# Kernel tuning notes

Hardware: AMD Instinct MI355X
Metric: run time of the kernel (lower is better)

Reference implementation:

```python
import jax, jax.numpy as jnp
import numpy as np

NUM_HEADS = 16  # config.num_attention_heads


def setup_inputs() -> dict:
    key = jax.random.key(0)
    k0, k1, k2 = jax.random.split(key, 3)
    B, S, D = 2, 2048, 2048
    hd = D // NUM_HEADS  # 128
    hidden_states = jax.random.normal(k0, (B, S, D), dtype=jnp.float32)
    c_attn_w = jax.random.normal(k1, (D + 2 * hd, D), dtype=jnp.float32) * 0.02
    c_attn_b = jnp.zeros((D + 2 * hd,), dtype=jnp.float32)
    c_proj_w = jax.random.normal(k2, (D, D), dtype=jnp.float32) * 0.02
    c_proj_b = jnp.zeros((D,), dtype=jnp.float32)
    return {
        "hidden_states": hidden_states,
        "c_attn_w": c_attn_w,
        "c_attn_b": c_attn_b,
        "c_proj_w": c_proj_w,
        "c_proj_b": c_proj_b,
    }


def reference(hidden_states, c_attn_w, c_attn_b, c_proj_w, c_proj_b):
    B, S, D = hidden_states.shape
    H = NUM_HEADS
    hd = D // H
    scale = hd ** -0.5

    # fused QKV projection: [B,S,D] -> [B,S,D+2*hd]
    qkv = hidden_states @ c_attn_w.T + c_attn_b
    # multi-query split: per-head Q, single shared K and V
    q = qkv[..., :D].reshape(B, S, H, hd)        # [B,S,H,hd]
    k = qkv[..., D:D + hd]                       # [B,S,hd]
    v = qkv[..., D + hd:]                        # [B,S,hd]

    # attention scores (full matrix materialized, like the baddbmm path)
    scores = jnp.einsum('bqhd,bkd->bhqk', q, k) * scale  # [B,H,S,S]
    causal = jnp.tril(jnp.ones((S, S), dtype=bool))
    scores = jnp.where(causal, scores, jnp.finfo(scores.dtype).min)
    attn = jax.nn.softmax(scores, axis=-1)

    # context: shared V broadcast across heads
    ctx = jnp.einsum('bhqk,bkd->bqhd', attn, v).reshape(B, S, D)
    out = ctx @ c_proj_w.T + c_proj_b
    return out
```

## Files before the change

kernel.cpp:

```cpp
#include <hip/hip_runtime.h>
#include <hip/hip_bf16.h>
#include <math.h>

typedef unsigned short u16;
typedef __attribute__((ext_vector_type(8))) __bf16 bf16x8;
typedef __attribute__((ext_vector_type(4))) float f32x4;

__device__ inline u16 f2bf(float f) {
  union { float f; unsigned u; } x; x.f = f;
  unsigned r = x.u + 0x7fffu + ((x.u >> 16) & 1u);
  return (u16)(r >> 16);
}

__device__ inline unsigned cvtpk(float lo, float hi) {
  unsigned r;
  asm("v_cvt_pk_bf16_f32 %0, %1, %2" : "=v"(r) : "v"(lo), "v"(hi));
  return r;
}

__device__ inline float fexp2(float x) {
  float r;
  asm("v_exp_f32 %0, %1" : "=v"(r) : "v"(x));
  return r;
}

__device__ inline void async16(const void* g, void* l) {
  __builtin_amdgcn_global_load_lds(
      (const __attribute__((address_space(1))) void*)g,
      (__attribute__((address_space(3))) void*)l, 16, 0, 0);
}

__global__ __launch_bounds__(256) void cast3_kernel(
    const float* __restrict__ hs, const float* __restrict__ aw,
    const float* __restrict__ pw, u16* __restrict__ hs_o,
    u16* __restrict__ aw_o, u16* __restrict__ pw_o) {
  int blk = blockIdx.x;
  const float* in;
  u16* out;
  int i;
  if (blk < 8192) {
    in = hs; out = hs_o; i = blk * 256 + threadIdx.x;
  } else if (blk < 12800) {
    in = aw; out = aw_o; i = (blk - 8192) * 256 + threadIdx.x;
  } else {
    in = pw; out = pw_o; i = (blk - 12800) * 256 + threadIdx.x;
  }
  float4 v = ((const float4*)in)[i];
  u16 o0 = f2bf(v.x), o1 = f2bf(v.y), o2 = f2bf(v.z), o3 = f2bf(v.w);
  unsigned lo = (unsigned)o0 | ((unsigned)o1 << 16);
  unsigned hi = (unsigned)o2 | ((unsigned)o3 << 16);
  ((uint2*)out)[i] = make_uint2(lo, hi);
}

__global__ __launch_bounds__(256) void vt_kernel(
    const u16* __restrict__ qkv, u16* __restrict__ vt) {
  __shared__ u16 tile[32][136];
  const int t = threadIdx.x;
  const int b = blockIdx.x >> 6;
  const int S0 = (blockIdx.x & 63) * 32;
  const int s_l = t >> 3, dg = t & 7;
  const u16* src = qkv + ((size_t)b * 2048 + S0 + s_l) * 2304 + 2176 + dg * 16;
  *(uint4*)&tile[s_l][dg * 16] = *(const uint4*)src;
  *(uint4*)&tile[s_l][dg * 16 + 8] = *(const uint4*)(src + 8);
  __syncthreads();
  const int d = t >> 1, sh = t & 1;
  u16 buf[16];
#pragma unroll
  for (int j = 0; j < 16; ++j) buf[j] = tile[sh * 16 + j][d];
  u16* dst = vt + ((size_t)b * 128 + d) * 2048 + S0 + sh * 16;
  *(uint4*)dst = *(uint4*)&buf[0];
  *(uint4*)(dst + 8) = *(uint4*)&buf[8];
}

template <bool BF16OUT>
__global__ __launch_bounds__(256) void gemm_bt(
    const u16* __restrict__ A, const u16* __restrict__ Bw,
    const float* __restrict__ bias, void* __restrict__ Cout,
    int M, int N, int K, int qcols, float qscale) {
  __shared__ u16 As[2][128 * 64];
  __shared__ u16 Bs[2][128 * 64];
  const int t = threadIdx.x;
  const int w = t >> 6;
  const int lane = t & 63;
  const int lq = lane >> 4, lr = lane & 15;

  int bx = blockIdx.x, by = blockIdx.y;
  const int gx = gridDim.x, gy = gridDim.y;
  if ((gx & 1) == 0 && (gy & 3) == 0) {
    const int cw = gx >> 1, ch = gy >> 2;
    int id = by * gx + bx;
    int xcd = id & 7, j = id >> 3;
    bx = (xcd & 1) * cw + j % cw;
    by = (xcd >> 1) * ch + j / cw;
  }

  const long brow = (long)by * 128;
  const long bcol = (long)bx * 128;
  const int wr = (w >> 1) * 64, wc = (w & 1) * 64;
  f32x4 acc[4][4] = {};

  int rA[4], cA[4];
#pragma unroll
  for (int it = 0; it < 4; ++it) {
    int ci = it * 256 + t;
    rA[it] = ci >> 3;
    cA[it] = (ci & 7) ^ (rA[it] & 7);
  }

  char* const AsB = (char*)&As[0][0];
  char* const BsB = (char*)&Bs[0][0];

  auto stage = [&](int buf, int kt) {
    char* ad = AsB + buf * 16384;
    char* bd = BsB + buf * 16384;
#pragma unroll
    for (int it = 0; it < 4; ++it) {
      const u16* srcA = A + (brow + rA[it]) * (long)K + kt + cA[it] * 8;
      async16(srcA, ad + (it * 256 + w * 64) * 16);
      const u16* srcB = Bw + (bcol + rA[it]) * (long)K + kt + cA[it] * 8;
      async16(srcB, bd + (it * 256 + w * 64) * 16);
    }
  };

  const int swz = ((lr & 4) << 4) + ((lq << 4) ^ ((lr & 3) << 4));
  const int aB0 = (wr + lr) * 128 + swz;
  const int bB0 = (wc + lr) * 128 + swz;
  const char* const a00 = AsB + aB0;
  const char* const a01 = AsB + (aB0 ^ 64);
  const char* const a10 = AsB + 16384 + aB0;
  const char* const a11 = AsB + 16384 + (aB0 ^ 64);
  const char* const b00 = BsB + bB0;
  const char* const b01 = BsB + (bB0 ^ 64);
  const char* const b10 = BsB + 16384 + bB0;
  const char* const b11 = BsB + 16384 + (bB0 ^ 64);

  auto computeK = [&](const char* a0, const char* a1, const char* b0,
                      const char* b1) {
    bf16x8 af[4], bfr[4];
#pragma unroll
    for (int m = 0; m < 4; ++m) af[m] = *(const bf16x8*)(a0 + m * 2048);
#pragma unroll
    for (int n = 0; n < 4; ++n) bfr[n] = *(const bf16x8*)(b0 + n * 2048);
#pragma unroll
    for (int m = 0; m < 4; ++m)
#pragma unroll
      for (int n = 0; n < 4; ++n)
        acc[m][n] = __builtin_amdgcn_mfma_f32_16x16x32_bf16(
            af[m], bfr[n], acc[m][n], 0, 0, 0);
#pragma unroll
    for (int m = 0; m < 4; ++m) af[m] = *(const bf16x8*)(a1 + m * 2048);
#pragma unroll
    for (int n = 0; n < 4; ++n) bfr[n] = *(const bf16x8*)(b1 + n * 2048);
#pragma unroll
    for (int m = 0; m < 4; ++m)
#pragma unroll
      for (int n = 0; n < 4; ++n)
        acc[m][n] = __builtin_amdgcn_mfma_f32_16x16x32_bf16(
            af[m], bfr[n], acc[m][n], 0, 0, 0);
  };

  stage(0, 0);
  __syncthreads();

  for (int kt = 0; kt < K; kt += 128) {
    if (kt + 64 < K) stage(1, kt + 64);
    computeK(a00, a01, b00, b01);
    __syncthreads();
    if (kt + 128 < K) stage(0, kt + 128);
    computeK(a10, a11, b10, b11);
    __syncthreads();
  }

#pragma unroll
  for (int m = 0; m < 4; ++m) {
    long row0 = brow + wr + m * 16 + lq * 4;
#pragma unroll
    for (int n = 0; n < 4; ++n) {
      long col = bcol + wc + n * 16 + lr;
      float bv = bias[col];
      float cs = (col < qcols) ? qscale : 1.f;
#pragma unroll
      for (int j = 0; j < 4; ++j) {
        float v = (acc[m][n][j] + bv) * cs;
        if (BF16OUT)
          ((u16*)Cout)[(row0 + j) * N + col] = f2bf(v);
        else
          ((float*)Cout)[(row0 + j) * N + col] = v;
      }
    }
  }
}

__global__ __launch_bounds__(256, 2) void attn_kernel(
    const u16* __restrict__ qkv, const u16* __restrict__ vt,
    u16* __restrict__ ctx) {
  __shared__ u16 Kl[2][64 * 136];
  __shared__ u16 Vl[2][128 * 72];
  __shared__ u16 Pl[4][16 * 72];

  const int t = threadIdx.x;
  const int w = t >> 6;
  const int lane = t & 63;
  const int lq = lane >> 4, lr = lane & 15;
  const int lkey = lq * 4;
  const int bid = blockIdx.x;
  const int qtid = bid >> 5;
  const int qt = (qtid < 8) ? (15 - qtid) : (qtid - 8);
  const int hb = bid & 31;
  const int h = hb & 15;
  const int b = hb >> 4;
  const int s0w = qt * 128 + w * 32;
  const size_t qb = (size_t)b * 2048 * 2304;

  bf16x8 qg[2][4];
#pragma unroll
  for (int s = 0; s < 2; ++s)
#pragma unroll
    for (int kc = 0; kc < 4; ++kc)
      qg[s][kc] = *(const bf16x8*)(qkv + qb +
                                   (size_t)(s0w + s * 16 + lr) * 2304 +
                                   h * 128 + kc * 32 + lq * 8);

  const u16* kp[5];
  const u16* vp[5];
#pragma unroll
  for (int ii = 0; ii < 5; ++ii) {
    int I = 4 * ii + w;
    {
      int pp = I * 1024 + lane * 16;
      int row = pp / 272;
      int rem = pp - row * 272;
      int ch = (rem < 256) ? (rem >> 4) : 0;
      if (row > 63) row = 63;
      kp[ii] = qkv + qb + (size_t)row * 2304 + 2048 + ch * 8;
    }
    {
      int pp = I * 1024 + lane * 16;
      int row = pp / 144;
      int rem = pp - row * 144;
      int ch = (rem < 128) ? (rem >> 4) : 0;
      if (row > 127) row = 127;
      vp[ii] = vt + ((size_t)b * 128 + row) * 2048 + ch * 8;
    }
  }
  char* const KlB = (char*)&Kl[0][0];
  char* const VlB = (char*)&Vl[0][0];

  auto stage = [&](int buf) {
    char* kd = KlB + buf * 17408;
    char* vd = VlB + buf * 18432;
#pragma unroll
    for (int ii = 0; ii < 5; ++ii) {
      int I = 4 * ii + w;
      if (I < 17) {
        async16(kp[ii], kd + I * 1024);
        kp[ii] += 64 * 2304;
      }
    }
#pragma unroll
    for (int ii = 0; ii < 5; ++ii) {
      int I = 4 * ii + w;
      if (I < 18) {
        async16(vp[ii], vd + I * 1024);
        vp[ii] += 64;
      }
    }
  };

  const int loK = lr * 272 + lq * 16;
  const int loV = lr * 144 + lq * 16;
  char* const pb = (char*)&Pl[w][0];
  char* const pw0 = pb + lr * 144 + lq * 8;
  const char* const PL = pb + lr * 144 + lq * 16;

  float mreg[2] = {-INFINITY, -INFINITY};
  float lreg[2] = {0.f, 0.f};
  f32x4 o[2][8] = {};
  const int ntiles = 2 * qt + 2;

  stage(0);
  __syncthreads();

  int cur = 0;
  for (int j2 = 0; j2 < ntiles; ++j2) {
    const int kvb = j2 * 64;
    if (j2 + 1 < ntiles) stage(cur ^ 1);
    if (kvb <= s0w + 31) {
      const char* KL = KlB + cur * 17408 + loK;
      const char* VL = VlB + cur * 18432 + loV;
      const bool maskT = (kvb + 63 > s0w);

      f32x4 sc[2][4] = {};
#pragma unroll
      for (int g = 0; g < 4; ++g)
#pragma unroll
        for (int kc = 0; kc < 4; ++kc) {
          bf16x8 kf = *(const bf16x8*)(KL + g * 4352 + kc * 64);
          sc[0][g] = __builtin_amdgcn_mfma_f32_16x16x32_bf16(kf, qg[0][kc],
                                                             sc[0][g], 0, 0, 0);
          sc[1][g] = __builtin_amdgcn_mfma_f32_16x16x32_bf16(kf, qg[1][kc],
                                                             sc[1][g], 0, 0, 0);
        }

      bf16x8 pa[2][2];
#pragma unroll
      for (int s = 0; s < 2; ++s) {
        float vv[16];
#pragma unroll
        for (int u = 0; u < 16; ++u) vv[u] = sc[s][u >> 2][u & 3];
        if (maskT) {
          const int qrel = s0w + s * 16 + lr - kvb;
#pragma unroll
          for (int g = 0; g < 4; ++g)
#pragma unroll
            for (int r = 0; r < 4; ++r)
              if (g * 16 + lkey + r > qrel) vv[g * 4 + r] = -INFINITY;
        }
        float mx = vv[0];
#pragma unroll
        for (int u = 1; u < 16; ++u) mx = fmaxf(mx, vv[u]);
        mx = fmaxf(mx, __shfl_xor(mx, 16));
        mx = fmaxf(mx, __shfl_xor(mx, 32));
        float mn = mreg[s];
        if (__any(mx > mn + 8.f)) {
          float mu = fmaxf(mn, mx);
          float alpha = fexp2(mn - mu);
          mreg[s] = mu;
          mn = mu;
          lreg[s] *= alpha;
          float a0 = __shfl(alpha, lkey + 0);
          float a1 = __shfl(alpha, lkey + 1);
          float a2 = __shfl(alpha, lkey + 2);
          float a3 = __shfl(alpha, lkey + 3);
#pragma unroll
          for (int n = 0; n < 8; ++n) {
            o[s][n][0] *= a0;
            o[s][n][1] *= a1;
            o[s][n][2] *= a2;
            o[s][n][3] *= a3;
          }
        }
        float rs = 0.f;
#pragma unroll
        for (int g = 0; g < 4; ++g)
#pragma unroll
          for (int rp = 0; rp < 2; ++rp) {
            float p0 = fexp2(vv[g * 4 + 2 * rp] - mn);
            float p1 = fexp2(vv[g * 4 + 2 * rp + 1] - mn);
            rs += p0 + p1;
            *(unsigned*)(pw0 + g * 32 + rp * 4) = cvtpk(p0, p1);
          }
        rs += __shfl_xor(rs, 16);
        rs += __shfl_xor(rs, 32);
        lreg[s] += rs;
        pa[s][0] = *(const bf16x8*)(PL);
        pa[s][1] = *(const bf16x8*)(PL + 64);
      }

#pragma unroll
      for (int n = 0; n < 8; ++n) {
        bf16x8 vf0 = *(const bf16x8*)(VL + n * 2304);
        bf16x8 vf1 = *(const bf16x8*)(VL + n * 2304 + 64);
        o[0][n] = __builtin_amdgcn_mfma_f32_16x16x32_bf16(pa[0][0], vf0,
                                                          o[0][n], 0, 0, 0);
        o[0][n] = __builtin_amdgcn_mfma_f32_16x16x32_bf16(pa[0][1], vf1,
                                                          o[0][n], 0, 0, 0);
        o[1][n] = __builtin_amdgcn_mfma_f32_16x16x32_bf16(pa[1][0], vf0,
                                                          o[1][n], 0, 0, 0);
        o[1][n] = __builtin_amdgcn_mfma_f32_16x16x32_bf16(pa[1][1], vf1,
                                                          o[1][n], 0, 0, 0);
      }
    }
    __syncthreads();
    cur ^= 1;
  }

#pragma unroll
  for (int s = 0; s < 2; ++s) {
    float inv = 1.f / lreg[s];
    float iv[4];
    iv[0] = __shfl(inv, lkey + 0);
    iv[1] = __shfl(inv, lkey + 1);
    iv[2] = __shfl(inv, lkey + 2);
    iv[3] = __shfl(inv, lkey + 3);
#pragma unroll
    for (int r = 0; r < 4; ++r) {
      size_t rowoff =
          ((size_t)b * 2048 + s0w + s * 16 + lkey + r) * 2048 + h * 128;
#pragma unroll
      for (int n = 0; n < 8; ++n)
        ctx[rowoff + n * 16 + lr] = f2bf(o[s][n][r] * iv[r]);
    }
  }
}

extern "C" void kernel_launch(void* const* d_in, const int* in_sizes, int n_in,
                              void* d_out, int out_size, void* d_ws,
                              size_t ws_size, hipStream_t stream) {
  (void)in_sizes; (void)n_in; (void)out_size; (void)ws_size;
  const float* hs = (const float*)d_in[0];
  const float* attn_w = (const float*)d_in[1];
  const float* attn_b = (const float*)d_in[2];
  const float* proj_w = (const float*)d_in[3];
  const float* proj_b = (const float*)d_in[4];
  float* out = (float*)d_out;

  u16* hs_b = (u16*)d_ws;
  u16* aw_b = hs_b + (size_t)4096 * 2048;
  u16* pw_b = aw_b + (size_t)2304 * 2048;
  u16* qkv_b = pw_b + (size_t)2048 * 2048;
  u16* vt_b = qkv_b + (size_t)4096 * 2304;
  u16* ctx_b = vt_b + (size_t)2 * 128 * 2048;

  const float qscale = 0.08838834764831845f * 1.4426950408889634f;

  cast3_kernel<<<16896, 256, 0, stream>>>(hs, attn_w, proj_w, hs_b, aw_b,
                                          pw_b);

  gemm_bt<true><<<dim3(18, 32), 256, 0, stream>>>(hs_b, aw_b, attn_b, qkv_b,
                                                  4096, 2304, 2048, 2048,
                                                  qscale);
  vt_kernel<<<128, 256, 0, stream>>>(qkv_b, vt_b);
  attn_kernel<<<512, 256, 0, stream>>>(qkv_b, vt_b, ctx_b);
  gemm_bt<false><<<dim3(16, 32), 256, 0, stream>>>(ctx_b, pw_b, proj_b, out,
                                                   4096, 2048, 2048, 0, 1.f);
}
```

Measured before the change: 185.3 us.

## Permute K rows in LDS so P stays in registers for PV MFMA

Reorders the key rows loaded into shared memory so that each lane's score-MFMA outputs line up with the A-operand layout the PV MFMA expects. The probabilities can then be packed to bf16 directly in registers, which removes the per-wave P staging buffer in LDS and its write-then-read round trip. The causal mask is rewritten to match the permuted key order. This lowers LDS traffic and waits, at the cost of more intricate index mapping, where any mistake would silently give wrong results.

```diff
diff --git a/kernel.cpp b/kernel.cpp
--- a/kernel.cpp
+++ b/kernel.cpp
@@ -196,13 +196,13 @@
     u16* __restrict__ ctx) {
   __shared__ u16 Kl[2][64 * 136];
   __shared__ u16 Vl[2][128 * 72];
-  __shared__ u16 Pl[4][16 * 72];
 
   const int t = threadIdx.x;
   const int w = t >> 6;
   const int lane = t & 63;
   const int lq = lane >> 4, lr = lane & 15;
   const int lkey = lq * 4;
+  const int kbase8 = lq << 3;
   const int bid = blockIdx.x;
   const int qtid = bid >> 5;
   const int qt = (qtid < 8) ? (15 - qtid) : (qtid - 8);
@@ -232,7 +232,10 @@
       int rem = pp - row * 272;
       int ch = (rem < 256) ? (rem >> 4) : 0;
       if (row > 63) row = 63;
-      kp[ii] = qkv + qb + (size_t)row * 2304 + 2048 + ch * 8;
+      int g = row >> 4, lqr = row & 15;
+      int key = ((g & 1) << 5) + ((lqr >> 2) << 3) + ((g >> 1) << 2) +
+                (lqr & 3);
+      kp[ii] = qkv + qb + (size_t)key * 2304 + 2048 + ch * 8;
     }
     {
       int pp = I * 1024 + lane * 16;
@@ -269,9 +272,6 @@
 
   const int loK = lr * 272 + lq * 16;
   const int loV = lr * 144 + lq * 16;
-  char* const pb = (char*)&Pl[w][0];
-  char* const pw0 = pb + lr * 144 + lq * 8;
-  const char* const PL = pb + lr * 144 + lq * 16;
 
   float mreg[2] = {-INFINITY, -INFINITY};
   float lreg[2] = {0.f, 0.f};
@@ -307,18 +307,19 @@
       for (int s = 0; s < 2; ++s) {
         float vv[16];
 #pragma unroll
-        for (int u = 0; u < 16; ++u) vv[u] = sc[s][u >> 2][u & 3];
+        for (int uu = 0; uu < 16; ++uu) vv[uu] = sc[s][uu >> 2][uu & 3];
         if (maskT) {
-          const int qrel = s0w + s * 16 + lr - kvb;
+          const int qrel = s0w + s * 16 + lr - kvb - kbase8;
 #pragma unroll
           for (int g = 0; g < 4; ++g)
 #pragma unroll
             for (int r = 0; r < 4; ++r)
-              if (g * 16 + lkey + r > qrel) vv[g * 4 + r] = -INFINITY;
+              if (((g & 1) << 5) + ((g >> 1) << 2) + r > qrel)
+                vv[g * 4 + r] = -INFINITY;
         }
         float mx = vv[0];
 #pragma unroll
-        for (int u = 1; u < 16; ++u) mx = fmaxf(mx, vv[u]);
+        for (int uu = 1; uu < 16; ++uu) mx = fmaxf(mx, vv[uu]);
         mx = fmaxf(mx, __shfl_xor(mx, 16));
         mx = fmaxf(mx, __shfl_xor(mx, 32));
         float mn = mreg[s];
@@ -340,21 +341,25 @@
             o[s][n][3] *= a3;
           }
         }
+        float e[16];
         float rs = 0.f;
 #pragma unroll
-        for (int g = 0; g < 4; ++g)
-#pragma unroll
-          for (int rp = 0; rp < 2; ++rp) {
-            float p0 = fexp2(vv[g * 4 + 2 * rp] - mn);
-            float p1 = fexp2(vv[g * 4 + 2 * rp + 1] - mn);
-            rs += p0 + p1;
-            *(unsigned*)(pw0 + g * 32 + rp * 4) = cvtpk(p0, p1);
-          }
+        for (int uu = 0; uu < 16; ++uu) {
+          e[uu] = fexp2(vv[uu] - mn);
+          rs += e[uu];
+        }
         rs += __shfl_xor(rs, 16);
         rs += __shfl_xor(rs, 32);
         lreg[s] += rs;
-        pa[s][0] = *(const bf16x8*)(PL);
-        pa[s][1] = *(const bf16x8*)(PL + 64);
+        union { unsigned uw[4]; bf16x8 v; } pk;
+#pragma unroll
+        for (int kc = 0; kc < 2; ++kc) {
+          pk.uw[0] = cvtpk(e[kc * 4 + 0], e[kc * 4 + 1]);
+          pk.uw[1] = cvtpk(e[kc * 4 + 2], e[kc * 4 + 3]);
+          pk.uw[2] = cvtpk(e[(kc + 2) * 4 + 0], e[(kc + 2) * 4 + 1]);
+          pk.uw[3] = cvtpk(e[(kc + 2) * 4 + 2], e[(kc + 2) * 4 + 3]);
+          pa[s][kc] = pk.v;
+        }
       }
 
 #pragma unroll
```

Measured after the change: 182.4 us. No clear change (-1.6%).
